# Kernel tuning notes

Measured on AMD Instinct MI355X. Metric: run time of the kernel, lower is better.

Reference implementation:

```python
import jax, jax.numpy as jnp
import numpy as np

N, E, G = 50000, 800000, 500
IN_DIM, EXTRA, HID, HEADS, NCLS = 128, 32, 64, 4, 1
NODE_FEAT2 = HID * HEADS  # 256, input to layer 2
FINAL = NODE_FEAT2 + EXTRA
NODES_PER_GRAPH = N // G  # 100


def gat_layer(h, W, a_l, a_r, b, src, dst, internal_relu):
    # DGL GATConv: fc -> per-head attn logits -> leaky_relu -> edge softmax (over dst) -> weighted sum
    feat = (h @ W).reshape(N, HEADS, HID)            # [N,H,D]
    el = jnp.sum(feat * a_l, axis=-1)                # [N,H]
    er = jnp.sum(feat * a_r, axis=-1)                # [N,H]
    e = jax.nn.leaky_relu(el[src] + er[dst], negative_slope=0.2)  # [E,H]
    m = jax.ops.segment_max(e, dst, num_segments=N)  # [N,H] (stable softmax)
    ex = jnp.exp(e - m[dst])
    denom = jax.ops.segment_sum(ex, dst, num_segments=N)
    alpha = ex / denom[dst]                          # [E,H]
    msg = feat[src] * alpha[:, :, None]              # [E,H,D]
    rst = jax.ops.segment_sum(msg, dst, num_segments=N) + b.reshape(1, HEADS, HID)
    if internal_relu:
        rst = jax.nn.relu(rst)
    return rst


def setup_inputs() -> dict:
    key = jax.random.key(0)
    ks = jax.random.split(key, 20)
    s = 0.05
    inp = {
        "x": jax.random.normal(ks[0], (N, IN_DIM), jnp.float32),
        "desc": jax.random.normal(ks[1], (G, EXTRA), jnp.float32),
        "src": jax.random.randint(ks[2], (E,), 0, N, jnp.int32),
        "dst": jax.random.randint(ks[3], (E,), 0, N, jnp.int32),
        "graph_id": (jnp.arange(N) // NODES_PER_GRAPH).astype(jnp.int32),
        # layer 1 params
        "W1": jax.random.normal(ks[4], (IN_DIM, HEADS * HID), jnp.float32) * s,
        "al1": jax.random.normal(ks[5], (HEADS, HID), jnp.float32) * s,
        "ar1": jax.random.normal(ks[6], (HEADS, HID), jnp.float32) * s,
        "b1": jnp.zeros((HEADS * HID,), jnp.float32),
        # layer 2 params
        "W2": jax.random.normal(ks[7], (NODE_FEAT2, HEADS * HID), jnp.float32) * s,
        "al2": jax.random.normal(ks[8], (HEADS, HID), jnp.float32) * s,
        "ar2": jax.random.normal(ks[9], (HEADS, HID), jnp.float32) * s,
        "b2": jnp.zeros((HEADS * HID,), jnp.float32),
        # MLP head (weights stored [in,out])
        "fc1_w": jax.random.normal(ks[10], (FINAL, HID), jnp.float32) * s,
        "fc1_b": jnp.zeros((HID,), jnp.float32),
        "fc2_w": jax.random.normal(ks[11], (HID, HID // 2), jnp.float32) * s,
        "fc2_b": jnp.zeros((HID // 2,), jnp.float32),
        "out_w": jax.random.normal(ks[12], (HID // 2, NCLS), jnp.float32) * s,
        "out_b": jnp.zeros((NCLS,), jnp.float32),
    }
    return inp


def reference(x, desc, src, dst, graph_id, W1, al1, ar1, b1, W2, al2, ar2, b2,
              fc1_w, fc1_b, fc2_w, fc2_b, out_w, out_b):
    h = gat_layer(x, W1, al1, ar1, b1, src, dst, internal_relu=True)
    h = jax.nn.relu(h.reshape(N, -1))                # flatten heads + outer relu (dropout=0)
    h = gat_layer(h, W2, al2, ar2, b2, src, dst, internal_relu=False)
    h = jax.nn.relu(h.reshape(N, -1))
    # dgl.mean_nodes over batched graph
    hg = jax.ops.segment_sum(h, graph_id, num_segments=G) / float(NODES_PER_GRAPH)  # [G, 256]
    combined = jnp.concatenate([hg, desc], axis=1)   # [G, 288]
    z = jax.nn.relu(combined @ fc1_w + fc1_b)
    z = jax.nn.relu(z @ fc2_w + fc2_b)
    return z @ out_w + out_b                          # [G, 1]
```

## Files before the change

kernel.cpp:

```cpp
#include <hip/hip_runtime.h>
#include <hip/hip_bf16.h>

#define N_NODES 50000
#define N_EDGES 800000
#define N_GRAPHS 500
#define IN_DIM 128
#define EXTRA 32
#define HID 64
#define HEADS 4
#define F2 256
#define NODES_PER_GRAPH 100
#define SCAN_BLOCKS ((N_NODES + 1023) / 1024)

typedef unsigned short u16;
typedef __attribute__((ext_vector_type(8))) short short8;
typedef __attribute__((ext_vector_type(4))) float floatx4;

__device__ __forceinline__ float bf2f(u16 u) {
    union { unsigned int i; float f; } v;
    v.i = ((unsigned int)u) << 16;
    return v.f;
}
__device__ __forceinline__ u16 f2b(float f) {
    __hip_bfloat16 h = __float2bfloat16(f);
    return *reinterpret_cast<u16*>(&h);
}

#define CNT_BLK 3125
#define CVT_BLK 6250
#define RP1_BLK 16
#define RP2_BLK 32
__global__ __launch_bounds__(256) void prep_kernel(const int* __restrict__ dst,
                                                   int* __restrict__ cnt,
                                                   const float* __restrict__ x,
                                                   u16* __restrict__ xb,
                                                   const float* __restrict__ W1,
                                                   u16* __restrict__ BF1,
                                                   const float* __restrict__ W2,
                                                   u16* __restrict__ BF2) {
    int b = blockIdx.x, t = threadIdx.x;
    if (b < CNT_BLK) {
        int e = b * 256 + t;
        if (e < N_EDGES) atomicAdd(&cnt[dst[e]], 1);
    } else if (b < CNT_BLK + CVT_BLK) {
        int i = (b - CNT_BLK) * 256 + t;
        float4 v = reinterpret_cast<const float4*>(x)[i];
        ushort4 o;
        o.x = f2b(v.x); o.y = f2b(v.y); o.z = f2b(v.z); o.w = f2b(v.w);
        reinterpret_cast<ushort4*>(xb)[i] = o;
    } else {
        const float* W;
        u16* BF;
        int chunk;
        if (b < CNT_BLK + CVT_BLK + RP1_BLK) {
            W = W1; BF = BF1; chunk = (b - CNT_BLK - CVT_BLK) * 4 + (t >> 6);
        } else {
            W = W2; BF = BF2; chunk = (b - CNT_BLK - CVT_BLK - RP1_BLK) * 4 + (t >> 6);
        }
        int l = t & 63;
        int kt = chunk >> 4, ct = chunk & 15;
        int col = ct * 16 + (l & 15);
        int k0 = kt * 32 + 8 * (l >> 4);
        u16* p = BF + (size_t)chunk * 512 + l * 8;
#pragma unroll
        for (int j = 0; j < 8; ++j) p[j] = f2b(W[(size_t)(k0 + j) * 256 + col]);
    }
}

__global__ __launch_bounds__(1024) void scan_block_kernel(const int* __restrict__ cnt,
                                                          int* __restrict__ part,
                                                          int* __restrict__ bsum) {
    __shared__ int buf[1024];
    int b = blockIdx.x, t = threadIdx.x;
    int i = b * 1024 + t;
    buf[t] = (i < N_NODES) ? cnt[i] : 0;
    __syncthreads();
    for (int d = 1; d < 1024; d <<= 1) {
        int add = (t >= d) ? buf[t - d] : 0;
        __syncthreads();
        buf[t] += add;
        __syncthreads();
    }
    if (i < N_NODES) part[i] = buf[t];
    if (t == 1023) bsum[b] = buf[t];
}

__global__ __launch_bounds__(1024) void scan_finalize_kernel(const int* __restrict__ part,
                                                             const int* __restrict__ bsum,
                                                             int* __restrict__ offs) {
    __shared__ int sbase;
    int t = threadIdx.x;
    if (t < 64) {
        int v = (t < blockIdx.x) ? bsum[t] : 0;
#pragma unroll
        for (int d = 32; d > 0; d >>= 1) v += __shfl_xor(v, d);
        if (t == 0) sbase = v;
    }
    __syncthreads();
    int i = blockIdx.x * 1024 + t;
    if (i < N_NODES) {
        offs[i + 1] = part[i] + sbase;
        if (i == 0) offs[0] = 0;
    }
}

__global__ void scatter_kernel(const int* __restrict__ src, const int* __restrict__ dst,
                               const int* __restrict__ offs, int* __restrict__ fill,
                               int* __restrict__ csr_src, int* __restrict__ csr_dst) {
    int e = blockIdx.x * blockDim.x + threadIdx.x;
    if (e >= N_EDGES) return;
    int s = src[e], d = dst[e];
    int pos = offs[d] + atomicAdd(&fill[d], 1);
    csr_src[pos] = s;
    csr_dst[pos] = d;
}

__global__ void edge_w_kernel(const int* __restrict__ csr_src, const int* __restrict__ csr_dst,
                              const float* __restrict__ el, const float* __restrict__ er,
                              float* __restrict__ w) {
    int p = blockIdx.x * blockDim.x + threadIdx.x;
    if (p >= N_EDGES) return;
    int s = csr_src[p], d = csr_dst[p];
    float4 l = *reinterpret_cast<const float4*>(&el[s * 4]);
    float4 r = *reinterpret_cast<const float4*>(&er[d * 4]);
    float4 o; float v;
    v = l.x + r.x; v = (v > 0.f) ? v : 0.2f * v; o.x = __expf(v);
    v = l.y + r.y; v = (v > 0.f) ? v : 0.2f * v; o.y = __expf(v);
    v = l.z + r.z; v = (v > 0.f) ? v : 0.2f * v; o.z = __expf(v);
    v = l.w + r.w; v = (v > 0.f) ? v : 0.2f * v; o.w = __expf(v);
    *reinterpret_cast<float4*>(&w[(size_t)p * 4]) = o;
}

template <int K>
__global__ __launch_bounds__(256) void gemm_mfma_attn_kernel(const u16* __restrict__ A,
                                                             const u16* __restrict__ BF,
                                                             const float* __restrict__ al,
                                                             const float* __restrict__ ar,
                                                             u16* __restrict__ C,
                                                             float* __restrict__ el,
                                                             float* __restrict__ er, int M) {
    const int NKT = K / 32;
    __shared__ u16 cxpose[4][16 * 68];
    int t = threadIdx.x;
    int wave = t >> 6, lane = t & 63;
    int l15 = lane & 15, kg = lane >> 4;
    int h = wave;
    int ct0 = h * 4;

    short8 breg[NKT][4];
#pragma unroll
    for (int kt = 0; kt < NKT; ++kt)
#pragma unroll
        for (int c = 0; c < 4; ++c)
            breg[kt][c] = *reinterpret_cast<const short8*>(
                              BF + (size_t)(kt * 16 + ct0 + c) * 512 + lane * 8);

    float alv[4], arv[4];
#pragma unroll
    for (int c = 0; c < 4; ++c) {
        alv[c] = al[(ct0 + c) * 16 + l15];
        arv[c] = ar[(ct0 + c) * 16 + l15];
    }

    u16* cbuf = cxpose[wave];
    for (int rt = 0; rt < 4; ++rt) {
        int row0 = blockIdx.x * 64 + rt * 16;
        if (row0 >= M) break;
        int arow = row0 + l15; if (arow >= M) arow = M - 1;
        const u16* Ap = A + (size_t)arow * K + kg * 8;

        floatx4 acc[4];
#pragma unroll
        for (int c = 0; c < 4; ++c) acc[c] = (floatx4)0.0f;
#pragma unroll
        for (int kt = 0; kt < NKT; ++kt) {
            short8 a = *reinterpret_cast<const short8*>(Ap + kt * 32);
#pragma unroll
            for (int c = 0; c < 4; ++c)
                acc[c] = __builtin_amdgcn_mfma_f32_16x16x32_bf16(a, breg[kt][c], acc[c], 0, 0, 0);
        }

        floatx4 pl = (floatx4)0.0f, pr = (floatx4)0.0f;
#pragma unroll
        for (int c = 0; c < 4; ++c) {
            pl += acc[c] * alv[c];
            pr += acc[c] * arv[c];
        }
#pragma unroll
        for (int off = 1; off < 16; off <<= 1) {
#pragma unroll
            for (int j = 0; j < 4; ++j) {
                pl[j] += __shfl_xor(pl[j], off);
                pr[j] += __shfl_xor(pr[j], off);
            }
        }
        if (l15 == 0) {
#pragma unroll
            for (int j = 0; j < 4; ++j) {
                int n = row0 + kg * 4 + j;
                if (n < M) { el[n * 4 + h] = pl[j]; er[n * 4 + h] = pr[j]; }
            }
        }

#pragma unroll
        for (int c = 0; c < 4; ++c)
#pragma unroll
            for (int j = 0; j < 4; ++j)
                cbuf[(kg * 4 + j) * 68 + c * 16 + l15] = f2b(acc[c][j]);
#pragma unroll
        for (int it = 0; it < 2; ++it) {
            int r = (lane >> 3) + it * 8;
            int cg = lane & 7;
            int grow = row0 + r;
            if (grow < M) {
                short8 v = *reinterpret_cast<const short8*>(cbuf + r * 68 + cg * 8);
                *reinterpret_cast<short8*>(C + (size_t)grow * 256 + h * 64 + cg * 8) = v;
            }
        }
    }
}

__global__ __launch_bounds__(256) void gather_kernel(const u16* __restrict__ feat,
                                                     const float* __restrict__ w,
                                                     const int* __restrict__ offs,
                                                     const int* __restrict__ csr_src,
                                                     const float* __restrict__ bias,
                                                     u16* __restrict__ outb) {
    int n = blockIdx.x * 4 + (threadIdx.x >> 6);
    if (n >= N_NODES) return;
    int lane = threadIdx.x & 63;
    int h = lane >> 4;
    const ushort4* feat4 = reinterpret_cast<const ushort4*>(feat);
    int s0 = offs[n], s1 = offs[n + 1];
    float4 acc = make_float4(0.f, 0.f, 0.f, 0.f);
    float den = 0.f;
    int i = s0;
    for (; i + 4 <= s1; i += 4) {
        int n0 = csr_src[i], n1 = csr_src[i + 1], n2 = csr_src[i + 2], n3 = csr_src[i + 3];
        float x0 = w[(size_t)(i + 0) * 4 + h];
        float x1 = w[(size_t)(i + 1) * 4 + h];
        float x2 = w[(size_t)(i + 2) * 4 + h];
        float x3 = w[(size_t)(i + 3) * 4 + h];
        ushort4 f0 = feat4[(size_t)n0 * 64 + lane];
        ushort4 f1 = feat4[(size_t)n1 * 64 + lane];
        ushort4 f2 = feat4[(size_t)n2 * 64 + lane];
        ushort4 f3 = feat4[(size_t)n3 * 64 + lane];
        acc.x = fmaf(x0, bf2f(f0.x), acc.x); acc.y = fmaf(x0, bf2f(f0.y), acc.y);
        acc.z = fmaf(x0, bf2f(f0.z), acc.z); acc.w = fmaf(x0, bf2f(f0.w), acc.w);
        acc.x = fmaf(x1, bf2f(f1.x), acc.x); acc.y = fmaf(x1, bf2f(f1.y), acc.y);
        acc.z = fmaf(x1, bf2f(f1.z), acc.z); acc.w = fmaf(x1, bf2f(f1.w), acc.w);
        acc.x = fmaf(x2, bf2f(f2.x), acc.x); acc.y = fmaf(x2, bf2f(f2.y), acc.y);
        acc.z = fmaf(x2, bf2f(f2.z), acc.z); acc.w = fmaf(x2, bf2f(f2.w), acc.w);
        acc.x = fmaf(x3, bf2f(f3.x), acc.x); acc.y = fmaf(x3, bf2f(f3.y), acc.y);
        acc.z = fmaf(x3, bf2f(f3.z), acc.z); acc.w = fmaf(x3, bf2f(f3.w), acc.w);
        den += (x0 + x1) + (x2 + x3);
    }
    for (; i < s1; ++i) {
        int s = csr_src[i];
        float x = w[(size_t)i * 4 + h];
        ushort4 f = feat4[(size_t)s * 64 + lane];
        acc.x = fmaf(x, bf2f(f.x), acc.x); acc.y = fmaf(x, bf2f(f.y), acc.y);
        acc.z = fmaf(x, bf2f(f.z), acc.z); acc.w = fmaf(x, bf2f(f.w), acc.w);
        den += x;
    }
    float inv = (s1 > s0) ? 1.f / den : 0.f;
    float4 bv = reinterpret_cast<const float4*>(bias)[lane];
    ushort4 o;
    o.x = f2b(fmaxf(fmaf(acc.x, inv, bv.x), 0.f));
    o.y = f2b(fmaxf(fmaf(acc.y, inv, bv.y), 0.f));
    o.z = f2b(fmaxf(fmaf(acc.z, inv, bv.z), 0.f));
    o.w = f2b(fmaxf(fmaf(acc.w, inv, bv.w), 0.f));
    reinterpret_cast<ushort4*>(outb)[(size_t)n * 64 + lane] = o;
}

__global__ __launch_bounds__(256) void head_kernel(const u16* __restrict__ h2,
                                                   const float* __restrict__ desc,
                                                   const float* __restrict__ fc1_w,
                                                   const float* __restrict__ fc1_b,
                                                   const float* __restrict__ fc2_w,
                                                   const float* __restrict__ fc2_b,
                                                   const float* __restrict__ out_w,
                                                   const float* __restrict__ out_b,
                                                   float* __restrict__ out) {
    __shared__ float comb[288];
    __shared__ float z1[64];
    __shared__ float z2[32];
    int g = blockIdx.x, t = threadIdx.x;
    const u16* base = h2 + (size_t)g * NODES_PER_GRAPH * 256;
    float s0 = 0.f, s1 = 0.f, s2 = 0.f, s3 = 0.f;
    for (int i = 0; i < NODES_PER_GRAPH; i += 4) {
        s0 += bf2f(base[(size_t)(i + 0) * 256 + t]);
        s1 += bf2f(base[(size_t)(i + 1) * 256 + t]);
        s2 += bf2f(base[(size_t)(i + 2) * 256 + t]);
        s3 += bf2f(base[(size_t)(i + 3) * 256 + t]);
    }
    comb[t] = ((s0 + s1) + (s2 + s3)) * (1.f / NODES_PER_GRAPH);
    if (t < EXTRA) comb[256 + t] = desc[g * EXTRA + t];
    __syncthreads();
    if (t < 64) {
        float a = fc1_b[t];
        for (int i = 0; i < 288; ++i) a += comb[i] * fc1_w[i * 64 + t];
        z1[t] = fmaxf(a, 0.f);
    }
    __syncthreads();
    if (t < 32) {
        float a = fc2_b[t];
        for (int i = 0; i < 64; ++i) a += z1[i] * fc2_w[i * 32 + t];
        z2[t] = fmaxf(a, 0.f);
    }
    __syncthreads();
    if (t == 0) {
        float a = out_b[0];
        for (int i = 0; i < 32; ++i) a += z2[i] * out_w[i];
        out[g] = a;
    }
}

extern "C" void kernel_launch(void* const* d_in, const int* in_sizes, int n_in,
                              void* d_out, int out_size, void* d_ws, size_t ws_size,
                              hipStream_t stream) {
    const float* x     = (const float*)d_in[0];
    const float* desc  = (const float*)d_in[1];
    const int*   src   = (const int*)d_in[2];
    const int*   dst   = (const int*)d_in[3];
    const float* W1    = (const float*)d_in[5];
    const float* al1   = (const float*)d_in[6];
    const float* ar1   = (const float*)d_in[7];
    const float* b1    = (const float*)d_in[8];
    const float* W2    = (const float*)d_in[9];
    const float* al2   = (const float*)d_in[10];
    const float* ar2   = (const float*)d_in[11];
    const float* b2    = (const float*)d_in[12];
    const float* fc1_w = (const float*)d_in[13];
    const float* fc1_b = (const float*)d_in[14];
    const float* fc2_w = (const float*)d_in[15];
    const float* fc2_b = (const float*)d_in[16];
    const float* out_w = (const float*)d_in[17];
    const float* out_b = (const float*)d_in[18];
    float* out = (float*)d_out;

    char* ws = (char*)d_ws;
    size_t off = 0;
    auto alloc = [&](size_t bytes) -> void* {
        void* p = ws + off;
        off = (off + bytes + 255) & ~(size_t)255;
        return p;
    };
    u16*   xb      = (u16*)alloc((size_t)N_NODES * IN_DIM * 2);
    u16*   featb   = (u16*)alloc((size_t)N_NODES * 256 * 2);
    u16*   h1b     = (u16*)alloc((size_t)N_NODES * 256 * 2);
    u16*   h2b     = (u16*)alloc((size_t)N_NODES * 256 * 2);
    u16*   BF1     = (u16*)alloc((size_t)IN_DIM * 256 * 2);
    u16*   BF2     = (u16*)alloc((size_t)F2 * 256 * 2);
    float* el      = (float*)alloc((size_t)N_NODES * 4 * 4);
    float* er      = (float*)alloc((size_t)N_NODES * 4 * 4);
    int*   offs    = (int*)alloc((size_t)(N_NODES + 1) * 4);
    int*   cntfill = (int*)alloc((size_t)2 * N_NODES * 4);
    int*   part    = (int*)alloc((size_t)N_NODES * 4);
    int*   bsum    = (int*)alloc(64 * 4);
    int*   csr_src = (int*)alloc((size_t)N_EDGES * 4);
    int*   csr_dst = (int*)alloc((size_t)N_EDGES * 4);
    float* wbuf    = (float*)alloc((size_t)N_EDGES * 4 * 4);
    int* cnt = cntfill, *fill = cntfill + N_NODES;

    hipMemsetAsync(cntfill, 0, (size_t)2 * N_NODES * 4, stream);
    prep_kernel<<<CNT_BLK + CVT_BLK + RP1_BLK + RP2_BLK, 256, 0, stream>>>(
        dst, cnt, x, xb, W1, BF1, W2, BF2);
    scan_block_kernel<<<SCAN_BLOCKS, 1024, 0, stream>>>(cnt, part, bsum);
    scan_finalize_kernel<<<SCAN_BLOCKS, 1024, 0, stream>>>(part, bsum, offs);
    scatter_kernel<<<(N_EDGES + 255) / 256, 256, 0, stream>>>(src, dst, offs, fill,
                                                              csr_src, csr_dst);

    int gb = (N_NODES + 63) / 64;
    int eb = (N_EDGES + 255) / 256;
    int ngb = (N_NODES + 3) / 4;
    gemm_mfma_attn_kernel<IN_DIM><<<gb, 256, 0, stream>>>(xb, BF1, al1, ar1, featb, el, er, N_NODES);
    edge_w_kernel<<<eb, 256, 0, stream>>>(csr_src, csr_dst, el, er, wbuf);
    gather_kernel<<<ngb, 256, 0, stream>>>(featb, wbuf, offs, csr_src, b1, h1b);
    gemm_mfma_attn_kernel<F2><<<gb, 256, 0, stream>>>(h1b, BF2, al2, ar2, featb, el, er, N_NODES);
    edge_w_kernel<<<eb, 256, 0, stream>>>(csr_src, csr_dst, el, er, wbuf);
    gather_kernel<<<ngb, 256, 0, stream>>>(featb, wbuf, offs, csr_src, b2, h2b);
    head_kernel<<<N_GRAPHS, 256, 0, stream>>>(h2b, desc, fc1_w, fc1_b, fc2_w, fc2_b,
                                              out_w, out_b, out);
}
```

Measured before the change: 296.7 us.

## Fuse CSR scatter into layer-1 GEMM launch and fill csr_dst from scan

Layer-1 GEMM/attention blocks and edge-scatter blocks now share one launch, interleaved one GEMM block per four scatter blocks, so the latency-bound atomic scatter overlaps the MFMA work and one kernel launch disappears. csr_dst is no longer written per edge by the scatter. The scan finalize kernel fills it by writing each node index across its CSR range. That per-thread loop is serial and unbalanced for high-degree nodes, and mixing block types can make scheduling uneven.

```diff
diff --git a/kernel.cpp b/kernel.cpp
--- a/kernel.cpp
+++ b/kernel.cpp
@@ -11,6 +11,8 @@
 #define F2 256
 #define NODES_PER_GRAPH 100
 #define SCAN_BLOCKS ((N_NODES + 1023) / 1024)
+#define GEMM1_BLKS 782
+#define SCAT_BLKS 3125
 
 typedef unsigned short u16;
 typedef __attribute__((ext_vector_type(8))) short short8;
@@ -87,32 +89,152 @@
 
 __global__ __launch_bounds__(1024) void scan_finalize_kernel(const int* __restrict__ part,
                                                              const int* __restrict__ bsum,
-                                                             int* __restrict__ offs) {
-    __shared__ int sbase;
+                                                             int* __restrict__ offs,
+                                                             int* __restrict__ csr_dst) {
+    __shared__ int sb;
     int t = threadIdx.x;
     if (t < 64) {
         int v = (t < blockIdx.x) ? bsum[t] : 0;
 #pragma unroll
         for (int d = 32; d > 0; d >>= 1) v += __shfl_xor(v, d);
-        if (t == 0) sbase = v;
+        if (t == 0) sb = v;
     }
     __syncthreads();
+    int sbase = sb;
     int i = blockIdx.x * 1024 + t;
     if (i < N_NODES) {
-        offs[i + 1] = part[i] + sbase;
+        int hi = part[i] + sbase;
+        offs[i + 1] = hi;
         if (i == 0) offs[0] = 0;
-    }
-}
-
-__global__ void scatter_kernel(const int* __restrict__ src, const int* __restrict__ dst,
-                               const int* __restrict__ offs, int* __restrict__ fill,
-                               int* __restrict__ csr_src, int* __restrict__ csr_dst) {
-    int e = blockIdx.x * blockDim.x + threadIdx.x;
-    if (e >= N_EDGES) return;
-    int s = src[e], d = dst[e];
-    int pos = offs[d] + atomicAdd(&fill[d], 1);
-    csr_src[pos] = s;
-    csr_dst[pos] = d;
+        int lo = (t == 0) ? sbase : part[i - 1] + sbase;
+        for (int p = lo; p < hi; ++p) csr_dst[p] = i;
+    }
+}
+
+template <int K>
+__device__ __forceinline__ void gemm_attn_body(int bx, const u16* __restrict__ A,
+                                               const u16* __restrict__ BF,
+                                               const float* __restrict__ al,
+                                               const float* __restrict__ ar,
+                                               u16* __restrict__ C,
+                                               float* __restrict__ el,
+                                               float* __restrict__ er, int M) {
+    const int NKT = K / 32;
+    __shared__ u16 cxpose[4][16 * 68];
+    int t = threadIdx.x;
+    int wave = t >> 6, lane = t & 63;
+    int l15 = lane & 15, kg = lane >> 4;
+    int h = wave;
+    int ct0 = h * 4;
+
+    short8 breg[NKT][4];
+#pragma unroll
+    for (int kt = 0; kt < NKT; ++kt)
+#pragma unroll
+        for (int c = 0; c < 4; ++c)
+            breg[kt][c] = *reinterpret_cast<const short8*>(
+                              BF + (size_t)(kt * 16 + ct0 + c) * 512 + lane * 8);
+
+    float alv[4], arv[4];
+#pragma unroll
+    for (int c = 0; c < 4; ++c) {
+        alv[c] = al[(ct0 + c) * 16 + l15];
+        arv[c] = ar[(ct0 + c) * 16 + l15];
+    }
+
+    u16* cbuf = cxpose[wave];
+    for (int rt = 0; rt < 4; ++rt) {
+        int row0 = bx * 64 + rt * 16;
+        if (row0 >= M) break;
+        int arow = row0 + l15; if (arow >= M) arow = M - 1;
+        const u16* Ap = A + (size_t)arow * K + kg * 8;
+
+        floatx4 acc[4];
+#pragma unroll
+        for (int c = 0; c < 4; ++c) acc[c] = (floatx4)0.0f;
+#pragma unroll
+        for (int kt = 0; kt < NKT; ++kt) {
+            short8 a = *reinterpret_cast<const short8*>(Ap + kt * 32);
+#pragma unroll
+            for (int c = 0; c < 4; ++c)
+                acc[c] = __builtin_amdgcn_mfma_f32_16x16x32_bf16(a, breg[kt][c], acc[c], 0, 0, 0);
+        }
+
+        floatx4 pl = (floatx4)0.0f, pr = (floatx4)0.0f;
+#pragma unroll
+        for (int c = 0; c < 4; ++c) {
+            pl += acc[c] * alv[c];
+            pr += acc[c] * arv[c];
+        }
+#pragma unroll
+        for (int off = 1; off < 16; off <<= 1) {
+#pragma unroll
+            for (int j = 0; j < 4; ++j) {
+                pl[j] += __shfl_xor(pl[j], off);
+                pr[j] += __shfl_xor(pr[j], off);
+            }
+        }
+        if (l15 == 0) {
+#pragma unroll
+            for (int j = 0; j < 4; ++j) {
+                int n = row0 + kg * 4 + j;
+                if (n < M) { el[n * 4 + h] = pl[j]; er[n * 4 + h] = pr[j]; }
+            }
+        }
+
+#pragma unroll
+        for (int c = 0; c < 4; ++c)
+#pragma unroll
+            for (int j = 0; j < 4; ++j)
+                cbuf[(kg * 4 + j) * 68 + c * 16 + l15] = f2b(acc[c][j]);
+#pragma unroll
+        for (int it = 0; it < 2; ++it) {
+            int r = (lane >> 3) + it * 8;
+            int cg = lane & 7;
+            int grow = row0 + r;
+            if (grow < M) {
+                short8 v = *reinterpret_cast<const short8*>(cbuf + r * 68 + cg * 8);
+                *reinterpret_cast<short8*>(C + (size_t)grow * 256 + h * 64 + cg * 8) = v;
+            }
+        }
+    }
+}
+
+__global__ __launch_bounds__(256) void gemm1_scatter_kernel(const u16* __restrict__ A,
+                                                            const u16* __restrict__ BF,
+                                                            const float* __restrict__ al,
+                                                            const float* __restrict__ ar,
+                                                            u16* __restrict__ C,
+                                                            float* __restrict__ el,
+                                                            float* __restrict__ er,
+                                                            const int* __restrict__ src,
+                                                            const int* __restrict__ dst,
+                                                            const int* __restrict__ offs,
+                                                            int* __restrict__ fill,
+                                                            int* __restrict__ csr_src) {
+    int b = blockIdx.x;
+    int g = b / 5, r = b - g * 5;
+    if (r == 0) {
+        gemm_attn_body<IN_DIM>(g, A, BF, al, ar, C, el, er, N_NODES);
+    } else {
+        int e = (b - g - 1) * 256 + threadIdx.x;
+        if (e < N_EDGES) {
+            int s = src[e], d = dst[e];
+            int pos = offs[d] + atomicAdd(&fill[d], 1);
+            csr_src[pos] = s;
+        }
+    }
+}
+
+template <int K>
+__global__ __launch_bounds__(256) void gemm_mfma_attn_kernel(const u16* __restrict__ A,
+                                                             const u16* __restrict__ BF,
+                                                             const float* __restrict__ al,
+                                                             const float* __restrict__ ar,
+                                                             u16* __restrict__ C,
+                                                             float* __restrict__ el,
+                                                             float* __restrict__ er, int M) {
+    gemm_attn_body<K>(blockIdx.x, A, BF, al, ar, C, el, er, M);
 }
 
 __global__ void edge_w_kernel(const int* __restrict__ csr_src, const int* __restrict__ csr_dst,
@@ -129,95 +251,6 @@
     v = l.z + r.z; v = (v > 0.f) ? v : 0.2f * v; o.z = __expf(v);
     v = l.w + r.w; v = (v > 0.f) ? v : 0.2f * v; o.w = __expf(v);
     *reinterpret_cast<float4*>(&w[(size_t)p * 4]) = o;
-}
-
-template <int K>
-__global__ __launch_bounds__(256) void gemm_mfma_attn_kernel(const u16* __restrict__ A,
-                                                             const u16* __restrict__ BF,
-                                                             const float* __restrict__ al,
-                                                             const float* __restrict__ ar,
-                                                             u16* __restrict__ C,
-                                                             float* __restrict__ el,
-                                                             float* __restrict__ er, int M) {
-    const int NKT = K / 32;
-    __shared__ u16 cxpose[4][16 * 68];
-    int t = threadIdx.x;
-    int wave = t >> 6, lane = t & 63;
-    int l15 = lane & 15, kg = lane >> 4;
-    int h = wave;
-    int ct0 = h * 4;
-
-    short8 breg[NKT][4];
-#pragma unroll
-    for (int kt = 0; kt < NKT; ++kt)
-#pragma unroll
-        for (int c = 0; c < 4; ++c)
-            breg[kt][c] = *reinterpret_cast<const short8*>(
-                              BF + (size_t)(kt * 16 + ct0 + c) * 512 + lane * 8);
-
-    float alv[4], arv[4];
-#pragma unroll
-    for (int c = 0; c < 4; ++c) {
-        alv[c] = al[(ct0 + c) * 16 + l15];
-        arv[c] = ar[(ct0 + c) * 16 + l15];
-    }
-
-    u16* cbuf = cxpose[wave];
-    for (int rt = 0; rt < 4; ++rt) {
-        int row0 = blockIdx.x * 64 + rt * 16;
-        if (row0 >= M) break;
-        int arow = row0 + l15; if (arow >= M) arow = M - 1;
-        const u16* Ap = A + (size_t)arow * K + kg * 8;
-
-        floatx4 acc[4];
-#pragma unroll
-        for (int c = 0; c < 4; ++c) acc[c] = (floatx4)0.0f;
-#pragma unroll
-        for (int kt = 0; kt < NKT; ++kt) {
-            short8 a = *reinterpret_cast<const short8*>(Ap + kt * 32);
-#pragma unroll
-            for (int c = 0; c < 4; ++c)
-                acc[c] = __builtin_amdgcn_mfma_f32_16x16x32_bf16(a, breg[kt][c], acc[c], 0, 0, 0);
-        }
-
-        floatx4 pl = (floatx4)0.0f, pr = (floatx4)0.0f;
-#pragma unroll
-        for (int c = 0; c < 4; ++c) {
-            pl += acc[c] * alv[c];
-            pr += acc[c] * arv[c];
-        }
-#pragma unroll
-        for (int off = 1; off < 16; off <<= 1) {
-#pragma unroll
-            for (int j = 0; j < 4; ++j) {
-                pl[j] += __shfl_xor(pl[j], off);
-                pr[j] += __shfl_xor(pr[j], off);
-            }
-        }
-        if (l15 == 0) {
-#pragma unroll
-            for (int j = 0; j < 4; ++j) {
-                int n = row0 + kg * 4 + j;
-                if (n < M) { el[n * 4 + h] = pl[j]; er[n * 4 + h] = pr[j]; }
-            }
-        }
-
-#pragma unroll
-        for (int c = 0; c < 4; ++c)
-#pragma unroll
-            for (int j = 0; j < 4; ++j)
-                cbuf[(kg * 4 + j) * 68 + c * 16 + l15] = f2b(acc[c][j]);
-#pragma unroll
-        for (int it = 0; it < 2; ++it) {
-            int r = (lane >> 3) + it * 8;
-            int cg = lane & 7;
-            int grow = row0 + r;
-            if (grow < M) {
-                short8 v = *reinterpret_cast<const short8*>(cbuf + r * 68 + cg * 8);
-                *reinterpret_cast<short8*>(C + (size_t)grow * 256 + h * 64 + cg * 8) = v;
-            }
-        }
-    }
 }
 
 __global__ __launch_bounds__(256) void gather_kernel(const u16* __restrict__ feat,
@@ -367,17 +400,16 @@
     prep_kernel<<<CNT_BLK + CVT_BLK + RP1_BLK + RP2_BLK, 256, 0, stream>>>(
         dst, cnt, x, xb, W1, BF1, W2, BF2);
     scan_block_kernel<<<SCAN_BLOCKS, 1024, 0, stream>>>(cnt, part, bsum);
-    scan_finalize_kernel<<<SCAN_BLOCKS, 1024, 0, stream>>>(part, bsum, offs);
-    scatter_kernel<<<(N_EDGES + 255) / 256, 256, 0, stream>>>(src, dst, offs, fill,
-                                                              csr_src, csr_dst);
-
-    int gb = (N_NODES + 63) / 64;
+    scan_finalize_kernel<<<SCAN_BLOCKS, 1024, 0, stream>>>(part, bsum, offs, csr_dst);
+
     int eb = (N_EDGES + 255) / 256;
     int ngb = (N_NODES + 3) / 4;
-    gemm_mfma_attn_kernel<IN_DIM><<<gb, 256, 0, stream>>>(xb, BF1, al1, ar1, featb, el, er, N_NODES);
+    gemm1_scatter_kernel<<<GEMM1_BLKS + SCAT_BLKS, 256, 0, stream>>>(
+        xb, BF1, al1, ar1, featb, el, er, src, dst, offs, fill, csr_src);
     edge_w_kernel<<<eb, 256, 0, stream>>>(csr_src, csr_dst, el, er, wbuf);
     gather_kernel<<<ngb, 256, 0, stream>>>(featb, wbuf, offs, csr_src, b1, h1b);
-    gemm_mfma_attn_kernel<F2><<<gb, 256, 0, stream>>>(h1b, BF2, al2, ar2, featb, el, er, N_NODES);
+    gemm_mfma_attn_kernel<F2><<<(N_NODES + 63) / 64, 256, 0, stream>>>(
+        h1b, BF2, al2, ar2, featb, el, er, N_NODES);
     edge_w_kernel<<<eb, 256, 0, stream>>>(csr_src, csr_dst, el, er, wbuf);
     gather_kernel<<<ngb, 256, 0, stream>>>(featb, wbuf, offs, csr_src, b2, h2b);
     head_kernel<<<N_GRAPHS, 256, 0, stream>>>(h2b, desc, fc1_w, fc1_b, fc2_w, fc2_b,
```

Measured after the change: 277.6 us. -6.4%, faster.
